# Kernel optimization log

Hardware: AMD Instinct MI355X
Metric: run time of the kernel (lower is better)

Reference implementation:

```python
import jax, jax.numpy as jnp
import numpy as np

N_WIRES = 4
# Fixed realization of tq.RandomLayer(n_ops=8, wires=[0..3]):
# a deterministic sequence of 8 parameterized gates with angles theta[k].
RANDOM_OPS = [
    ("rx", (0,)), ("ry", (1,)), ("rz", (3,)), ("crx", (0, 2)),
    ("ry", (3,)), ("rx", (2,)), ("crx", (1, 3)), ("rz", (0,)),
]


def _ry(t):
    c = jnp.cos(t / 2).astype(jnp.complex64)
    s = jnp.sin(t / 2).astype(jnp.complex64)
    return jnp.stack([jnp.stack([c, -s]), jnp.stack([s, c])])


def _rx(t):
    c = jnp.cos(t / 2).astype(jnp.complex64)
    s = jnp.sin(t / 2).astype(jnp.complex64)
    return jnp.stack([jnp.stack([c, -1j * s]), jnp.stack([-1j * s, c])])


def _rz(t):
    e0 = jnp.exp(-1j * (t / 2)).astype(jnp.complex64)
    e1 = jnp.exp(1j * (t / 2)).astype(jnp.complex64)
    z = jnp.zeros((), jnp.complex64)
    return jnp.stack([jnp.stack([e0, z]), jnp.stack([z, e1])])


def _crx(t):
    U = _rx(t)
    z2 = jnp.zeros((2, 2), jnp.complex64)
    i2 = jnp.eye(2, dtype=jnp.complex64)
    return jnp.concatenate([jnp.concatenate([i2, z2], 1), jnp.concatenate([z2, U], 1)], 0)


def _apply_1q(psi, U, w):
    # psi: (N,2,2,2,2); apply 2x2 gate on wire w
    psi = jnp.moveaxis(psi, 1 + w, -1)
    psi = psi @ U.T
    return jnp.moveaxis(psi, -1, 1 + w)


def _apply_2q(psi, U4, w1, w2):
    psi = jnp.moveaxis(psi, (1 + w1, 1 + w2), (-2, -1))
    shp = psi.shape
    psi = (psi.reshape(shp[:-2] + (4,)) @ U4.T).reshape(shp)
    return jnp.moveaxis(psi, (-2, -1), (1 + w1, 1 + w2))


def _quanv_forward(x, theta, W, b):
    B = x.shape[0]
    img = x.reshape(B, 28, 28)
    # 2x2 stride-2 patches, order [x[r,c], x[r,c+1], x[r+1,c], x[r+1,c+1]]
    patches = img.reshape(B, 14, 2, 14, 2).transpose(0, 1, 3, 2, 4).reshape(B * 196, 4)
    # RY-encoded product state: ry(a)|0> = [cos(a/2), sin(a/2)]
    half = patches * 0.5
    c = jnp.cos(half).astype(jnp.complex64)
    s = jnp.sin(half).astype(jnp.complex64)
    v = jnp.stack([c, s], axis=-1)  # (N, 4 wires, 2)
    psi = jnp.einsum('na,nb,nc,nd->nabcd', v[:, 0], v[:, 1], v[:, 2], v[:, 3])
    gate_fns = {"rx": _rx, "ry": _ry, "rz": _rz}
    for k, (name, wires) in enumerate(RANDOM_OPS):
        t = theta[k]
        if name == "crx":
            psi = _apply_2q(psi, _crx(t), wires[0], wires[1])
        else:
            psi = _apply_1q(psi, gate_fns[name](t), wires[0])
    probs = (psi.real ** 2 + psi.imag ** 2).reshape(-1, 16)  # (N,16)
    # PauliZ expectation per wire; wire 0 is the most significant bit
    idx = jnp.arange(16)
    bits = (idx[:, None] >> (3 - jnp.arange(N_WIRES)[None, :])) & 1
    z_table = (1.0 - 2.0 * bits).astype(jnp.float32)  # (16,4)
    meas = probs @ z_table  # (N,4)
    feats = meas.reshape(B, 196 * 4)  # (B,784), patch-major like torch.cat
    logits = feats @ W.T + b
    return jax.nn.log_softmax(logits, axis=-1)


def setup_inputs() -> dict:
    key = jax.random.key(0)
    k1, k2, k3 = jax.random.split(key, 3)
    B = 2048
    x = jax.random.normal(k1, (B, 1, 28, 28), jnp.float32)
    theta = jax.random.normal(k2, (8,), jnp.float32)
    W = jax.random.normal(k3, (10, 784), jnp.float32) * 0.02
    b = jnp.zeros((10,), jnp.float32)
    return {"x": x, "theta": theta, "W": W, "b": b}


def reference(x, theta, W, b):
    return _quanv_forward(x, theta, W, b)
```

## Files before the change

kernel.cpp:

```cpp
#include <hip/hip_runtime.h>
#include <math.h>


__global__ __launch_bounds__(256) void quanv_fused_kernel(
    const float* __restrict__ xin,
    const float* __restrict__ theta,
    const float* __restrict__ Wm,
    const float* __restrict__ bv,
    float* __restrict__ out,
    int B)
{
    const int t = threadIdx.x;
    const int w = t >> 6, l = t & 63;
    const int img = blockIdx.x * 4 + w;
    if (img >= B) return;

    const float* ib = xin + (size_t)img * 784;
    const bool tail = (l < 4);

    float2 rA[4], rB[4];
#pragma unroll
    for (int k = 0; k < 3; ++k) {
        const int p = l + 64 * k;
        const int pi = p / 14, pj = p % 14;
        const float* pr = ib + pi * 56 + pj * 2;
        rA[k] = *(const float2*)pr;
        rB[k] = *(const float2*)(pr + 28);
    }
    {
        const int p = tail ? (192 + l) : l;
        const int pi = p / 14, pj = p % 14;
        const float* pr = ib + pi * 56 + pj * 2;
        rA[3] = *(const float2*)pr;
        rB[3] = *(const float2*)(pr + 28);
    }

    const float t0 = theta[0], th1 = theta[1], t2 = theta[2], t3 = theta[3];
    const float t4 = theta[4], t5 = theta[5], t6 = theta[6];
    const float c5g = cosf(t5), c35 = cosf(t3 + t5);
    const float c6 = cosf(t6), s6 = sinf(t6);
    const float k0 = cosf(t0);
    const float A  = 0.5f * (c5g + c35);
    const float Bc = 0.5f * k0 * (c5g - c35);
    const float C1 = 0.5f * (1.f + c6);
    const float C2 = 0.5f * (1.f - c6);
    const float K1 = cosf(t4);
    const float K2 = -sinf(t4) * cosf(t2);
    const float C5 = 0.5f * s6 * sinf(t2);

    auto featf = [&](float2 a, float2 b) -> float4 {
        const float ca0 = __cosf(a.x);
        const float u   = __cosf(a.y + th1);
        const float ca2 = __cosf(b.x);
        float sa3, ca3;
        __sincosf(b.y, &sa3, &ca3);
        const float m0 = k0 * ca0;
        const float m2 = ca2 * fmaf(Bc, ca0, A);
        const float zu = fmaf(K1, ca3, K2 * sa3);
        const float m3 = fmaf(fmaf(C2, u, C1), zu, C5 * sa3 * (1.f - u));
        return make_float4(m0, u, m2, m3);
    };

    float acc[10];
#pragma unroll
    for (int c = 0; c < 10; ++c) acc[c] = 0.f;

    const float4* W4 = (const float4*)Wm;
#pragma unroll
    for (int k = 0; k < 3; ++k) {
        const float4 f = featf(rA[k], rB[k]);
        const int p = l + 64 * k;
#pragma unroll
        for (int c = 0; c < 10; ++c) {
            const float4 wv = W4[c * 196 + p];
            acc[c] = fmaf(f.w, wv.w, fmaf(f.z, wv.z,
                     fmaf(f.y, wv.y, fmaf(f.x, wv.x, acc[c]))));
        }
    }
    if (tail) {
        const float4 f = featf(rA[3], rB[3]);
        const int p = 192 + l;
#pragma unroll
        for (int c = 0; c < 10; ++c) {
            const float4 wv = W4[c * 196 + p];
            acc[c] = fmaf(f.w, wv.w, fmaf(f.z, wv.z,
                     fmaf(f.y, wv.y, fmaf(f.x, wv.x, acc[c]))));
        }
    }

    float logit[10];
#pragma unroll
    for (int c = 0; c < 10; ++c) {
        float v = acc[c];
        v += __shfl_xor(v, 32, 64);
        v += __shfl_xor(v, 16, 64);
        v += __shfl_xor(v, 8, 64);
        v += __shfl_xor(v, 4, 64);
        v += __shfl_xor(v, 2, 64);
        v += __shfl_xor(v, 1, 64);
        logit[c] = v + bv[c];
    }

    float mx = -1e30f;
#pragma unroll
    for (int c = 0; c < 10; ++c) mx = fmaxf(mx, logit[c]);
    float sum = 0.f;
#pragma unroll
    for (int c = 0; c < 10; ++c) sum += __expf(logit[c] - mx);
    const float ls = __logf(sum);

    if (l < 10) {
        float v = logit[9];
#pragma unroll
        for (int c = 8; c >= 0; --c) v = (l == c) ? logit[c] : v;
        out[(size_t)img * 10 + l] = v - mx - ls;
    }
}

extern "C" void kernel_launch(void* const* d_in, const int* in_sizes, int n_in,
                              void* d_out, int out_size, void* d_ws, size_t ws_size,
                              hipStream_t stream) {
    const float* x     = (const float*)d_in[0];
    const float* theta = (const float*)d_in[1];
    const float* W     = (const float*)d_in[2];
    const float* bias  = (const float*)d_in[3];
    float* out         = (float*)d_out;

    const int B = in_sizes[0] / 784;
    const int grid = (B + 3) / 4;
    quanv_fused_kernel<<<grid, 256, 0, stream>>>(x, theta, W, bias, out, B);
}
```

Measured before the change: 10.71 us.

## Use DPP wave reduction, fast intrinsics for theta trig, predicate tail loads

Replaces the shuffle-based butterfly reduction of the ten class accumulators with a DPP row-shift and row-broadcast reduction followed by readlane from lane 63. This avoids the LDS-backed ds_bpermute traffic that shuffles compile to. The per-thread setup trig on theta switches from precise cosf/sinf to the fast __cosf/__sinf intrinsics, and the tail patch loads now happen only on the lanes that use them. The trade-off is lower accuracy in the theta-derived constants, plus reliance on gfx9-specific DPP row_bcast controls being correct on this architecture.

New measurement: 10.47 us, median of 2. 2.2% less time.

```diff
diff --git a/kernel.cpp b/kernel.cpp
--- a/kernel.cpp
+++ b/kernel.cpp
@@ -1,6 +1,20 @@
 #include <hip/hip_runtime.h>
 #include <math.h>
 
+
+__device__ __forceinline__ float wave_sum_dpp(float v) {
+#define DPP_ADD(CTRL, RMASK)                                                  \
+    v += __int_as_float(__builtin_amdgcn_update_dpp(                          \
+        0, __float_as_int(v), (CTRL), (RMASK), 0xf, true))
+    DPP_ADD(0x111, 0xf);
+    DPP_ADD(0x112, 0xf);
+    DPP_ADD(0x114, 0xf);
+    DPP_ADD(0x118, 0xf);
+    DPP_ADD(0x142, 0xa);
+    DPP_ADD(0x143, 0xc);
+#undef DPP_ADD
+    return __int_as_float(__builtin_amdgcn_readlane(__float_as_int(v), 63));
+}
 
 __global__ __launch_bounds__(256) void quanv_fused_kernel(
     const float* __restrict__ xin,
@@ -27,8 +41,8 @@
         rA[k] = *(const float2*)pr;
         rB[k] = *(const float2*)(pr + 28);
     }
-    {
-        const int p = tail ? (192 + l) : l;
+    if (tail) {
+        const int p = 192 + l;
         const int pi = p / 14, pj = p % 14;
         const float* pr = ib + pi * 56 + pj * 2;
         rA[3] = *(const float2*)pr;
@@ -37,16 +51,16 @@
 
     const float t0 = theta[0], th1 = theta[1], t2 = theta[2], t3 = theta[3];
     const float t4 = theta[4], t5 = theta[5], t6 = theta[6];
-    const float c5g = cosf(t5), c35 = cosf(t3 + t5);
-    const float c6 = cosf(t6), s6 = sinf(t6);
-    const float k0 = cosf(t0);
+    const float c5g = __cosf(t5), c35 = __cosf(t3 + t5);
+    const float c6 = __cosf(t6), s6 = __sinf(t6);
+    const float k0 = __cosf(t0);
     const float A  = 0.5f * (c5g + c35);
     const float Bc = 0.5f * k0 * (c5g - c35);
     const float C1 = 0.5f * (1.f + c6);
     const float C2 = 0.5f * (1.f - c6);
-    const float K1 = cosf(t4);
-    const float K2 = -sinf(t4) * cosf(t2);
-    const float C5 = 0.5f * s6 * sinf(t2);
+    const float K1 = __cosf(t4);
+    const float K2 = -__sinf(t4) * __cosf(t2);
+    const float C5 = 0.5f * s6 * __sinf(t2);
 
     auto featf = [&](float2 a, float2 b) -> float4 {
         const float ca0 = __cosf(a.x);
@@ -90,16 +104,7 @@
 
     float logit[10];
 #pragma unroll
-    for (int c = 0; c < 10; ++c) {
-        float v = acc[c];
-        v += __shfl_xor(v, 32, 64);
-        v += __shfl_xor(v, 16, 64);
-        v += __shfl_xor(v, 8, 64);
-        v += __shfl_xor(v, 4, 64);
-        v += __shfl_xor(v, 2, 64);
-        v += __shfl_xor(v, 1, 64);
-        logit[c] = v + bv[c];
-    }
+    for (int c = 0; c < 10; ++c) logit[c] = wave_sum_dpp(acc[c]) + bv[c];
 
     float mx = -1e30f;
 #pragma unroll
```
